# Kernel tuning notes

Measured on AMD Instinct MI355X. Metric: run time of the kernel, lower is better.

Reference implementation:

```python
import jax, jax.numpy as jnp
import numpy as np

DEPTH_REF = jnp.array([28.01, 16.32], dtype=jnp.float32)
DIM_REF = jnp.array([[3.88, 1.63, 1.53], [0.84, 1.76, 0.66], [1.78, 1.52, 1.78]], dtype=jnp.float32)
TOPK = 50
DET_THRESHOLD = 0.25
PI = 3.14159265358979


def nms_hm(heat, kernel=3):
    # 3x3 max-pool NMS: keep peaks, zero everything else
    pad = (kernel - 1) // 2
    hmax = jax.lax.reduce_window(heat, -jnp.inf, jax.lax.max,
                                 (1, 1, kernel, kernel), (1, 1, 1, 1),
                                 [(0, 0), (0, 0), (pad, pad), (pad, pad)])
    return jnp.where(hmax == heat, heat, 0.0)


def select_topk(heat, K):
    B, C, H, W = heat.shape
    scores_all, inds_all = jax.lax.top_k(heat.reshape(B, C, H * W), K)  # [B,C,K]
    ys_all = (inds_all // W).astype(jnp.float32)
    xs_all = (inds_all % W).astype(jnp.float32)
    scores, inds = jax.lax.top_k(scores_all.reshape(B, C * K), K)       # [B,K] over classes
    clses = (inds // K).astype(jnp.float32)
    topk_inds = jnp.take_along_axis(inds_all.reshape(B, C * K), inds, axis=1)
    ys = jnp.take_along_axis(ys_all.reshape(B, C * K), inds, axis=1)
    xs = jnp.take_along_axis(xs_all.reshape(B, C * K), inds, axis=1)
    return scores, topk_inds, clses, ys, xs


def select_point_of_interest(index, feature_maps):
    B, Cf, H, W = feature_maps.shape
    fm = feature_maps.transpose(0, 2, 3, 1).reshape(B, H * W, Cf)
    return jnp.take_along_axis(fm, index[:, :, None], axis=1)  # [B,K,Cf]


def encode_box3d(rotys, dims, locs):
    # dims = (l, h, w); corner signs reproduce SMOKE's gather pattern
    N = rotys.shape[0]
    c, s = jnp.cos(rotys), jnp.sin(rotys)
    z, o = jnp.zeros_like(c), jnp.ones_like(c)
    ry = jnp.stack([c, z, s, z, o, z, -s, z, c], axis=1).reshape(N, 3, 3)
    sx = jnp.array([-0.5, 0.5, 0.5, 0.5, 0.5, -0.5, -0.5, -0.5], dtype=dims.dtype)
    sy = jnp.array([-1., -1., 0., 0., -1., -1., 0., 0.], dtype=dims.dtype)
    sz = jnp.array([-0.5, -0.5, -0.5, 0.5, 0.5, 0.5, 0.5, -0.5], dtype=dims.dtype)
    corners = jnp.stack([dims[:, 0:1] * sx, dims[:, 1:2] * sy, dims[:, 2:3] * sz], axis=1)  # [N,3,8]
    return jnp.einsum('nij,njk->nik', ry, corners) + locs[:, :, None]


def setup_inputs() -> dict:
    key = jax.random.key(0)
    k1, k2 = jax.random.split(key)
    B, C, H, W = 32, 3, 192, 640
    IMG_W, IMG_H = 4 * W, 4 * H
    pred_heatmap = jax.random.uniform(k1, (B, C, H, W), dtype=jnp.float32)
    pred_regression = jax.random.normal(k2, (B, 8, H, W), dtype=jnp.float32) * 0.5
    # affine image->heatmap (scale 1/4), invertible
    tm = jnp.array([[0.25, 0., 0.], [0., 0.25, 0.], [0., 0., 1.]], dtype=jnp.float32)
    trans_mat = jnp.tile(tm[None], (B, 1, 1))
    Kc = jnp.array([[721.5, 0., IMG_W / 2.], [0., 721.5, IMG_H / 2.], [0., 0., 1.]], dtype=jnp.float32)
    K_mat = jnp.tile(Kc[None], (B, 1, 1))
    img_size = jnp.tile(jnp.array([[IMG_W, IMG_H]], dtype=jnp.float32), (B, 1))
    return {"pred_heatmap": pred_heatmap, "pred_regression": pred_regression,
            "trans_mat": trans_mat, "K_mat": K_mat, "img_size": img_size}


def reference(pred_heatmap, pred_regression, trans_mat, K_mat, img_size):
    B = pred_heatmap.shape[0]
    heat = nms_hm(pred_heatmap)
    scores, inds, clses, ys, xs = select_topk(heat, TOPK)
    reg = select_point_of_interest(inds, pred_regression).reshape(-1, 8)  # [B*K,8]

    points = jnp.stack([xs.reshape(-1), ys.reshape(-1)], axis=1)          # heatmap coords
    depth_off, proj_off = reg[:, 0], reg[:, 1:3]
    dim_off, ori = reg[:, 3:6], reg[:, 6:8]
    cls_idx = clses.reshape(-1).astype(jnp.int32)

    obj_id = jnp.repeat(jnp.arange(B), TOPK)
    tm_inv = jnp.linalg.inv(trans_mat)[obj_id]   # [N,3,3]
    K_inv = jnp.linalg.inv(K_mat)[obj_id]

    # decode location: heatmap -> image -> camera frame
    proj = points + proj_off
    proj_ext = jnp.concatenate([proj, jnp.ones_like(proj[:, :1])], axis=1)
    proj_img = jnp.einsum('nij,nj->ni', tm_inv, proj_ext)                 # image-plane homog coords
    depths = depth_off * DEPTH_REF[1] + DEPTH_REF[0]
    locs = jnp.einsum('nij,nj->ni', K_inv, proj_img * depths[:, None])

    dims = jnp.exp(dim_off) * DIM_REF[cls_idx]                            # (l,h,w)
    locs = locs.at[:, 1].add(dims[:, 1] / 2)

    # decode orientation
    eps = 1e-7
    rays = jnp.arctan(locs[:, 0] / (locs[:, 2] + eps))
    alphas = jnp.arctan(ori[:, 0] / (ori[:, 1] + eps))
    alphas = jnp.where(ori[:, 1] >= 0, alphas - PI / 2, alphas + PI / 2)
    rotys = alphas + rays
    wrap = lambda a: jnp.where(a > PI, a - 2 * PI, jnp.where(a < -PI, a + 2 * PI, a))
    rotys, alphas = wrap(rotys), wrap(alphas)

    # encode 2D boxes from projected 3D corners
    corners = encode_box3d(rotys, dims, locs)                             # [N,3,8]
    proj2 = jnp.einsum('nij,njk->nik', K_mat[obj_id], corners)
    xy = proj2[:, :2] / proj2[:, 2:3]
    Wi, Hi = img_size[obj_id, 0], img_size[obj_id, 1]
    xmins = jnp.clip(xy[:, 0].min(axis=1), 0.0, Wi)
    ymins = jnp.clip(xy[:, 1].min(axis=1), 0.0, Hi)
    xmaxs = jnp.clip(xy[:, 0].max(axis=1), 0.0, Wi)
    ymaxs = jnp.clip(xy[:, 1].max(axis=1), 0.0, Hi)
    box2d = jnp.stack([xmins, ymins, xmaxs, ymaxs], axis=1)

    dims_rolled = jnp.roll(dims, -1, axis=1)                              # (h,w,l)
    result = jnp.concatenate([
        cls_idx.astype(jnp.float32)[:, None], alphas[:, None], box2d,
        dims_rolled, locs, rotys[:, None], scores.reshape(-1, 1)], axis=1)  # [B*K,14]
    keep = result[:, -1] > DET_THRESHOLD
    return jnp.where(keep[:, None], result, 0.0)
```

## Files before the change

kernel.cpp:

```cpp
#include <hip/hip_runtime.h>
#include <math.h>

#define Hd 192
#define Wd 640
#define HWp (Hd * Wd)
#define NCLS 3
#define KTOP 50
#define NB 32
#define NPL (NB * NCLS)
#define GPR 160
#define GPP (HWp / 4)
#define SEGBLK 120
#define SEGCAP 32
#define CAP 2048
#define RBK 256
#define PI_F 3.14159265358979f

template <typename F>
__device__ inline void peaks_in_group(const float* __restrict__ p, int g, F&& f) {
  const int y = g / GPR;
  const int x0 = (g - y * GPR) * 4;
  const float* rm = p + y * Wd + x0;
  const float4 mq = *(const float4*)rm;
  const float ml = (x0 > 0) ? rm[-1] : -INFINITY;
  const float mr = (x0 + 4 < Wd) ? rm[4] : -INFINITY;
  float4 tq; float tl, tr;
  if (y > 0) {
    const float* rt = rm - Wd;
    tq = *(const float4*)rt;
    tl = (x0 > 0) ? rt[-1] : -INFINITY;
    tr = (x0 + 4 < Wd) ? rt[4] : -INFINITY;
  } else {
    tq.x = tq.y = tq.z = tq.w = -INFINITY; tl = -INFINITY; tr = -INFINITY;
  }
  float4 bq; float bl, br;
  if (y < Hd - 1) {
    const float* rb = rm + Wd;
    bq = *(const float4*)rb;
    bl = (x0 > 0) ? rb[-1] : -INFINITY;
    br = (x0 + 4 < Wd) ? rb[4] : -INFINITY;
  } else {
    bq.x = bq.y = bq.z = bq.w = -INFINITY; bl = -INFINITY; br = -INFINITY;
  }
  const float c0 = fmaxf(fmaxf(tl, ml), bl);
  const float c1 = fmaxf(fmaxf(tq.x, mq.x), bq.x);
  const float c2 = fmaxf(fmaxf(tq.y, mq.y), bq.y);
  const float c3 = fmaxf(fmaxf(tq.z, mq.z), bq.z);
  const float c4 = fmaxf(fmaxf(tq.w, mq.w), bq.w);
  const float c5 = fmaxf(fmaxf(tr, mr), br);
  const int base = y * Wd + x0;
  if (mq.x == fmaxf(fmaxf(c0, c1), c2)) f(__float_as_uint(mq.x), base + 0);
  if (mq.y == fmaxf(fmaxf(c1, c2), c3)) f(__float_as_uint(mq.y), base + 1);
  if (mq.z == fmaxf(fmaxf(c2, c3), c4)) f(__float_as_uint(mq.z), base + 2);
  if (mq.w == fmaxf(fmaxf(c3, c4), c5)) f(__float_as_uint(mq.w), base + 3);
}

template <typename F>
__device__ inline void for_each_peak_plane(const float* __restrict__ p, int tid,
                                           int nth, F&& f) {
  for (int g = tid; g < GPP; g += nth) peaks_in_group(p, g, f);
}

__device__ inline unsigned long long mk_key(unsigned int bits, int idx) {
  return ((unsigned long long)bits << 32) | (unsigned int)~idx;
}

__device__ inline int bucket_of(unsigned int bits) {
  const unsigned int base = __float_as_uint(0.995f);
  if (bits <= base) return 0;
  unsigned int d = (bits - base) >> 9;
  return d > 255u ? 255 : (int)d;
}

__global__ __launch_bounds__(256) void scan_kernel(
    const float* __restrict__ heat,
    int* __restrict__ counts,
    unsigned long long* __restrict__ segkey) {
  const int blk = blockIdx.x;
  const int plane = blk / SEGBLK;
  const int sub = blk - plane * SEGBLK;
  __shared__ unsigned long long s_k[SEGCAP];
  __shared__ int s_n;
  if (threadIdx.x == 0) s_n = 0;
  __syncthreads();

  const float* p = heat + (size_t)plane * HWp;
  const int g = sub * 256 + threadIdx.x;
  const unsigned int TB = __float_as_uint(0.995f);
  peaks_in_group(p, g, [&](unsigned int bits, int idx) {
    if (bits >= TB) {
      int slot = atomicAdd(&s_n, 1);
      if (slot < SEGCAP) s_k[slot] = mk_key(bits, idx);
    }
  });
  __syncthreads();
  const int n = s_n;
  if (threadIdx.x == 0) counts[blk] = n;
  const int nn = n < SEGCAP ? n : SEGCAP;
  if (threadIdx.x < nn)
    segkey[(size_t)blk * SEGCAP + threadIdx.x] = s_k[threadIdx.x];
}

__device__ inline void inv3(const float* m, float* o) {
  float a = m[0], b = m[1], c = m[2];
  float d = m[3], e = m[4], f = m[5];
  float g = m[6], h = m[7], i = m[8];
  float A = e * i - f * h;
  float B = -(d * i - f * g);
  float C = d * h - e * g;
  float det = a * A + b * B + c * C;
  float id = 1.0f / det;
  o[0] = A * id;            o[1] = -(b * i - c * h) * id; o[2] = (b * f - c * e) * id;
  o[3] = B * id;            o[4] = (a * i - c * g) * id;  o[5] = -(a * f - c * d) * id;
  o[6] = C * id;            o[7] = -(a * h - b * g) * id; o[8] = (a * e - b * d) * id;
}

__device__ inline float wrap_pi(float a) {
  if (a > PI_F) return a - 2.0f * PI_F;
  if (a < -PI_F) return a + 2.0f * PI_F;
  return a;
}

__constant__ float DIM_REF_C[9] = {3.88f, 1.63f, 1.53f,
                                   0.84f, 1.76f, 0.66f,
                                   1.78f, 1.52f, 1.78f};

__global__ __launch_bounds__(256) void rank_decode_kernel(
    const float* __restrict__ heat,
    const int* __restrict__ counts,
    const unsigned long long* __restrict__ segkey,
    const float* __restrict__ regr,
    const float* __restrict__ trans_mat,
    const float* __restrict__ K_mat,
    const float* __restrict__ img_size,
    float* __restrict__ out) {
  const int b = blockIdx.x;
  const int tid = threadIdx.x;

  __shared__ unsigned long long s_key[CAP];
  __shared__ unsigned long long g_key[CAP];
  __shared__ int s_off[SEGBLK + 1];
  __shared__ int cnt[RBK], suf[RBK], cur[RBK];
  __shared__ unsigned int fb_hist[1024];
  __shared__ float cls_sc[NCLS * KTOP];
  __shared__ int cls_pi[NCLS * KTOP];
  __shared__ int sel[KTOP];
  __shared__ int s_flag, s_cnt, s_B, s_above, s_T;

  for (int c = 0; c < NCLS; ++c) {
    const int plane = b * NCLS + c;
    __syncthreads();
    if (tid == 0) { s_flag = 0; s_off[0] = 0; }
    __syncthreads();
    if (tid < SEGBLK) {
      int n = counts[plane * SEGBLK + tid];
      if (n > SEGCAP) { atomicOr(&s_flag, 1); n = SEGCAP; }
      s_off[tid + 1] = n;
    }
    __syncthreads();
    if (tid == 0) {
      int acc = 0;
      for (int i = 1; i <= SEGBLK; ++i) { acc += s_off[i]; s_off[i] = acc; }
    }
    __syncthreads();
    int M = s_off[SEGBLK];
    const bool fast = (s_flag == 0) && (M >= KTOP) && (M <= CAP);

    if (fast) {
      if (tid < SEGBLK) {
        const int o = s_off[tid];
        const int n = s_off[tid + 1] - o;
        const unsigned long long* sk = segkey + (size_t)(plane * SEGBLK + tid) * SEGCAP;
        for (int i = 0; i < n; ++i) s_key[o + i] = sk[i];
      }
      __syncthreads();
    } else {
      const float* p = heat + (size_t)plane * HWp;
      for (int i = tid; i < 1024; i += 256) fb_hist[i] = 0;
      __syncthreads();
      for_each_peak_plane(p, tid, 256, [&](unsigned int bits, int idx) {
        unsigned int bkt = bits >> 20; if (bkt > 1023u) bkt = 1023u;
        atomicAdd(&fb_hist[bkt], 1u);
      });
      __syncthreads();
      if (tid == 0) {
        int acc = 0, Bs = -1;
        for (int bkt = 1023; bkt >= 0; --bkt) {
          int cc = (int)fb_hist[bkt];
          if (acc + cc >= KTOP) { Bs = bkt; s_above = acc; break; }
          acc += cc;
        }
        s_B = Bs;
        if (Bs < 0) s_above = acc;
      }
      __syncthreads();
      const int Bs = s_B;
      unsigned int T;
      if (Bs < 0) {
        T = 0;
      } else {
        for (int i = tid; i < 1024; i += 256) fb_hist[i] = 0;
        __syncthreads();
        for_each_peak_plane(p, tid, 256, [&](unsigned int bits, int idx) {
          unsigned int bkt = bits >> 20; if (bkt > 1023u) bkt = 1023u;
          if ((int)bkt == Bs) atomicAdd(&fb_hist[(bits >> 10) & 1023], 1u);
        });
        __syncthreads();
        if (tid == 0) {
          int acc = s_above, Ss = 0;
          for (int sb = 1023; sb >= 0; --sb) {
            int cc = (int)fb_hist[sb];
            if (acc + cc >= KTOP) { Ss = sb; break; }
            acc += cc;
          }
          s_T = (int)(((unsigned int)Bs << 20) | ((unsigned int)Ss << 10));
        }
        __syncthreads();
        T = (unsigned int)s_T;
      }
      if (tid == 0) s_cnt = 0;
      __syncthreads();
      for_each_peak_plane(p, tid, 256, [&](unsigned int bits, int idx) {
        if (bits >= T) {
          int slot = atomicAdd(&s_cnt, 1);
          if (slot < CAP) s_key[slot] = mk_key(bits, idx);
        }
      });
      __syncthreads();
      M = s_cnt < CAP ? s_cnt : CAP;
    }

    for (int i = tid; i < RBK; i += 256) { cnt[i] = 0; cur[i] = 0; }
    __syncthreads();
    for (int i = tid; i < M; i += 256)
      atomicAdd(&cnt[bucket_of((unsigned int)(s_key[i] >> 32))], 1);
    __syncthreads();
    if (tid == 0) {
      int acc = 0;
      for (int bq = RBK - 1; bq >= 0; --bq) { suf[bq] = acc; acc += cnt[bq]; }
    }
    __syncthreads();
    for (int i = tid; i < M; i += 256) {
      const unsigned long long k = s_key[i];
      const int bq = bucket_of((unsigned int)(k >> 32));
      const int slot = suf[bq] + atomicAdd(&cur[bq], 1);
      g_key[slot] = k;
    }
    __syncthreads();
    for (int i = tid; i < M; i += 256) {
      const unsigned long long k = g_key[i];
      const int bq = bucket_of((unsigned int)(k >> 32));
      const int st = suf[bq];
      const int nb = cnt[bq];
      int rank = st;
      for (int t = st; t < st + nb; ++t) rank += (g_key[t] > k);
      if (rank < KTOP) {
        cls_sc[c * KTOP + rank] = __uint_as_float((unsigned int)(k >> 32));
        cls_pi[c * KTOP + rank] = (int)~((unsigned int)k);
      }
    }
    for (int s2 = M + tid; s2 < KTOP; s2 += 256) {
      cls_sc[c * KTOP + s2] = 0.0f;
      cls_pi[c * KTOP + s2] = 0;
    }
  }
  __syncthreads();

  if (tid < NCLS * KTOP) {
    const float v = cls_sc[tid];
    int rank = 0;
    for (int j = 0; j < NCLS * KTOP; ++j) {
      const float w = cls_sc[j];
      rank += (w > v) || (w == v && j < tid);
    }
    if (rank < KTOP) sel[rank] = tid;
  }
  __syncthreads();

  if (tid < KTOP) {
    const int i = sel[tid];
    const int cls = i / KTOP;
    const float score = cls_sc[i];
    const int ind = cls_pi[i];
    const float ys = (float)(ind / Wd);
    const float xs = (float)(ind - (ind / Wd) * Wd);

    const float* rb = regr + (size_t)b * 8 * HWp + ind;
    const float r0 = rb[0 * HWp], r1 = rb[1 * HWp], r2 = rb[2 * HWp], r3 = rb[3 * HWp];
    const float r4 = rb[4 * HWp], r5 = rb[5 * HWp], r6 = rb[6 * HWp], r7 = rb[7 * HWp];

    float tm[9], km[9], tmi[9], kmi[9];
#pragma unroll
    for (int q = 0; q < 9; ++q) { tm[q] = trans_mat[b * 9 + q]; km[q] = K_mat[b * 9 + q]; }
    inv3(tm, tmi);
    inv3(km, kmi);

    const float px = xs + r1, py = ys + r2;
    const float gx = tmi[0] * px + tmi[1] * py + tmi[2];
    const float gy = tmi[3] * px + tmi[4] * py + tmi[5];
    const float gz = tmi[6] * px + tmi[7] * py + tmi[8];
    const float depth = r0 * 16.32f + 28.01f;
    const float qx = gx * depth, qy = gy * depth, qz = gz * depth;
    const float lx = kmi[0] * qx + kmi[1] * qy + kmi[2] * qz;
    float ly = kmi[3] * qx + kmi[4] * qy + kmi[5] * qz;
    const float lz = kmi[6] * qx + kmi[7] * qy + kmi[8] * qz;

    const float d0 = expf(r3) * DIM_REF_C[cls * 3 + 0];
    const float d1 = expf(r4) * DIM_REF_C[cls * 3 + 1];
    const float d2 = expf(r5) * DIM_REF_C[cls * 3 + 2];
    ly += d1 * 0.5f;

    const float ray = atanf(lx / (lz + 1e-7f));
    float alpha = atanf(r6 / (r7 + 1e-7f));
    alpha += (r7 >= 0.0f) ? -PI_F * 0.5f : PI_F * 0.5f;
    const float roty = wrap_pi(alpha + ray);
    alpha = wrap_pi(alpha);

    const float SX[8] = {-0.5f, 0.5f, 0.5f, 0.5f, 0.5f, -0.5f, -0.5f, -0.5f};
    const float SY[8] = {-1.0f, -1.0f, 0.0f, 0.0f, -1.0f, -1.0f, 0.0f, 0.0f};
    const float SZ[8] = {-0.5f, -0.5f, -0.5f, 0.5f, 0.5f, 0.5f, 0.5f, -0.5f};
    const float cr = cosf(roty), sr = sinf(roty);
    float minx = INFINITY, maxx = -INFINITY, miny = INFINITY, maxy = -INFINITY;
#pragma unroll
    for (int j = 0; j < 8; ++j) {
      const float ax = d0 * SX[j], ay = d1 * SY[j], az = d2 * SZ[j];
      const float cx = cr * ax + sr * az + lx;
      const float cy = ay + ly;
      const float cz = -sr * ax + cr * az + lz;
      const float ppx = km[0] * cx + km[1] * cy + km[2] * cz;
      const float ppy = km[3] * cx + km[4] * cy + km[5] * cz;
      const float ppz = km[6] * cx + km[7] * cy + km[8] * cz;
      const float X = ppx / ppz, Y = ppy / ppz;
      minx = fminf(minx, X); maxx = fmaxf(maxx, X);
      miny = fminf(miny, Y); maxy = fmaxf(maxy, Y);
    }
    const float Wi = img_size[b * 2 + 0], Hi = img_size[b * 2 + 1];
    const float xmin = fminf(fmaxf(minx, 0.0f), Wi);
    const float ymin = fminf(fmaxf(miny, 0.0f), Hi);
    const float xmax = fminf(fmaxf(maxx, 0.0f), Wi);
    const float ymax = fminf(fmaxf(maxy, 0.0f), Hi);

    float* o = out + (size_t)(b * KTOP + tid) * 14;
    if (score > 0.25f) {
      o[0] = (float)cls; o[1] = alpha;
      o[2] = xmin; o[3] = ymin; o[4] = xmax; o[5] = ymax;
      o[6] = d1; o[7] = d2; o[8] = d0;
      o[9] = lx; o[10] = ly; o[11] = lz;
      o[12] = roty; o[13] = score;
    } else {
#pragma unroll
      for (int q = 0; q < 14; ++q) o[q] = 0.0f;
    }
  }
}


extern "C" void kernel_launch(void* const* d_in, const int* in_sizes, int n_in,
                              void* d_out, int out_size, void* d_ws, size_t ws_size,
                              hipStream_t stream) {
  const float* heat = (const float*)d_in[0];
  const float* regr = (const float*)d_in[1];
  const float* tmat = (const float*)d_in[2];
  const float* kmat = (const float*)d_in[3];
  const float* isz = (const float*)d_in[4];

  char* ws = (char*)d_ws;
  int* counts = (int*)ws;
  unsigned long long* segkey = (unsigned long long*)(ws + 46080);

  scan_kernel<<<NPL * SEGBLK, 256, 0, stream>>>(heat, counts, segkey);
  rank_decode_kernel<<<NB, 256, 0, stream>>>(heat, counts, segkey,
                                             regr, tmat, kmat, isz, (float*)d_out);
}
```

Before: 226.6 us.

## Scan 16-wide strips per thread and parallelize segment key compaction

The scan kernel now has each thread handle a 16-pixel strip instead of a 4-pixel group. Neighbouring column maxima are shared across the strip, and the threshold test is checked before the peak comparison. This cuts the block count from 120 to 30 per plane and raises the per-segment capacity to 64. The rank kernel copies segment keys using all threads in a strided loop instead of one serial loop per segment. In exchange, each thread uses more registers and fewer blocks are launched, and a denser segment is more likely to overflow into the slow fallback path.

```diff
diff --git a/kernel.cpp b/kernel.cpp
--- a/kernel.cpp
+++ b/kernel.cpp
@@ -10,11 +10,17 @@
 #define NPL (NB * NCLS)
 #define GPR 160
 #define GPP (HWp / 4)
-#define SEGBLK 120
-#define SEGCAP 32
+#define SPR 40
+#define SPP (Hd * SPR)
+#define SEGBLK 30
+#define SEGCAP 64
 #define CAP 2048
 #define RBK 256
 #define PI_F 3.14159265358979f
+
+__device__ inline float fmax3(float a, float b, float c) {
+  return fmaxf(fmaxf(a, b), c);
+}
 
 template <typename F>
 __device__ inline void peaks_in_group(const float* __restrict__ p, int g, F&& f) {
@@ -42,17 +48,17 @@
   } else {
     bq.x = bq.y = bq.z = bq.w = -INFINITY; bl = -INFINITY; br = -INFINITY;
   }
-  const float c0 = fmaxf(fmaxf(tl, ml), bl);
-  const float c1 = fmaxf(fmaxf(tq.x, mq.x), bq.x);
-  const float c2 = fmaxf(fmaxf(tq.y, mq.y), bq.y);
-  const float c3 = fmaxf(fmaxf(tq.z, mq.z), bq.z);
-  const float c4 = fmaxf(fmaxf(tq.w, mq.w), bq.w);
-  const float c5 = fmaxf(fmaxf(tr, mr), br);
+  const float c0 = fmax3(tl, ml, bl);
+  const float c1 = fmax3(tq.x, mq.x, bq.x);
+  const float c2 = fmax3(tq.y, mq.y, bq.y);
+  const float c3 = fmax3(tq.z, mq.z, bq.z);
+  const float c4 = fmax3(tq.w, mq.w, bq.w);
+  const float c5 = fmax3(tr, mr, br);
   const int base = y * Wd + x0;
-  if (mq.x == fmaxf(fmaxf(c0, c1), c2)) f(__float_as_uint(mq.x), base + 0);
-  if (mq.y == fmaxf(fmaxf(c1, c2), c3)) f(__float_as_uint(mq.y), base + 1);
-  if (mq.z == fmaxf(fmaxf(c2, c3), c4)) f(__float_as_uint(mq.z), base + 2);
-  if (mq.w == fmaxf(fmaxf(c3, c4), c5)) f(__float_as_uint(mq.w), base + 3);
+  if (mq.x == fmax3(c0, c1, c2)) f(__float_as_uint(mq.x), base + 0);
+  if (mq.y == fmax3(c1, c2, c3)) f(__float_as_uint(mq.y), base + 1);
+  if (mq.z == fmax3(c2, c3, c4)) f(__float_as_uint(mq.z), base + 2);
+  if (mq.w == fmax3(c3, c4, c5)) f(__float_as_uint(mq.w), base + 3);
 }
 
 template <typename F>
@@ -70,6 +76,37 @@
   if (bits <= base) return 0;
   unsigned int d = (bits - base) >> 9;
   return d > 255u ? 255 : (int)d;
+}
+
+struct Row16 {
+  float4 q0, q1, q2, q3;
+  float l, r;
+};
+
+__device__ inline Row16 load_row16(const float* __restrict__ rp, int x0, bool valid) {
+  Row16 o;
+  if (valid) {
+    o.q0 = *(const float4*)(rp);
+    o.q1 = *(const float4*)(rp + 4);
+    o.q2 = *(const float4*)(rp + 8);
+    o.q3 = *(const float4*)(rp + 12);
+    o.l = (x0 > 0) ? rp[-1] : -INFINITY;
+    o.r = (x0 + 16 < Wd) ? rp[16] : -INFINITY;
+  } else {
+    o.q0.x = o.q0.y = o.q0.z = o.q0.w = -INFINITY;
+    o.q1 = o.q0; o.q2 = o.q0; o.q3 = o.q0;
+    o.l = -INFINITY; o.r = -INFINITY;
+  }
+  return o;
+}
+
+__device__ inline float4 max3v(const float4 a, const float4 b, const float4 c) {
+  float4 o;
+  o.x = fmax3(a.x, b.x, c.x);
+  o.y = fmax3(a.y, b.y, c.y);
+  o.z = fmax3(a.z, b.z, c.z);
+  o.w = fmax3(a.w, b.w, c.w);
+  return o;
 }
 
 __global__ __launch_bounds__(256) void scan_kernel(
@@ -84,15 +121,47 @@
   if (threadIdx.x == 0) s_n = 0;
   __syncthreads();
 
-  const float* p = heat + (size_t)plane * HWp;
-  const int g = sub * 256 + threadIdx.x;
-  const unsigned int TB = __float_as_uint(0.995f);
-  peaks_in_group(p, g, [&](unsigned int bits, int idx) {
-    if (bits >= TB) {
-      int slot = atomicAdd(&s_n, 1);
-      if (slot < SEGCAP) s_k[slot] = mk_key(bits, idx);
-    }
-  });
+  const int strip = sub * 256 + threadIdx.x;
+  const int y = strip / SPR;
+  const int x0 = (strip - y * SPR) * 16;
+  const float* pm = heat + (size_t)plane * HWp + y * Wd + x0;
+
+  const Row16 m = load_row16(pm, x0, true);
+  const Row16 t = load_row16(pm - Wd, x0, y > 0);
+  const Row16 b = load_row16(pm + Wd, x0, y < Hd - 1);
+
+  const float cl = fmax3(t.l, m.l, b.l);
+  const float cr = fmax3(t.r, m.r, b.r);
+  const float4 c0 = max3v(t.q0, m.q0, b.q0);
+  const float4 c1 = max3v(t.q1, m.q1, b.q1);
+  const float4 c2 = max3v(t.q2, m.q2, b.q2);
+  const float4 c3 = max3v(t.q3, m.q3, b.q3);
+
+  const float TH = 0.995f;
+  const int base = y * Wd + x0;
+#define EMIT(V, W0, W1, W2, J)                                         \
+  if ((V) >= TH && (V) == fmax3((W0), (W1), (W2))) {                   \
+    int slot = atomicAdd(&s_n, 1);                                     \
+    if (slot < SEGCAP) s_k[slot] = mk_key(__float_as_uint(V), base + (J)); \
+  }
+  EMIT(m.q0.x, cl,   c0.x, c0.y, 0)
+  EMIT(m.q0.y, c0.x, c0.y, c0.z, 1)
+  EMIT(m.q0.z, c0.y, c0.z, c0.w, 2)
+  EMIT(m.q0.w, c0.z, c0.w, c1.x, 3)
+  EMIT(m.q1.x, c0.w, c1.x, c1.y, 4)
+  EMIT(m.q1.y, c1.x, c1.y, c1.z, 5)
+  EMIT(m.q1.z, c1.y, c1.z, c1.w, 6)
+  EMIT(m.q1.w, c1.z, c1.w, c2.x, 7)
+  EMIT(m.q2.x, c1.w, c2.x, c2.y, 8)
+  EMIT(m.q2.y, c2.x, c2.y, c2.z, 9)
+  EMIT(m.q2.z, c2.y, c2.z, c2.w, 10)
+  EMIT(m.q2.w, c2.z, c2.w, c3.x, 11)
+  EMIT(m.q3.x, c2.w, c3.x, c3.y, 12)
+  EMIT(m.q3.y, c3.x, c3.y, c3.z, 13)
+  EMIT(m.q3.z, c3.y, c3.z, c3.w, 14)
+  EMIT(m.q3.w, c3.z, c3.w, cr,   15)
+#undef EMIT
+
   __syncthreads();
   const int n = s_n;
   if (threadIdx.x == 0) counts[blk] = n;
@@ -167,11 +236,13 @@
     const bool fast = (s_flag == 0) && (M >= KTOP) && (M <= CAP);
 
     if (fast) {
-      if (tid < SEGBLK) {
-        const int o = s_off[tid];
-        const int n = s_off[tid + 1] - o;
-        const unsigned long long* sk = segkey + (size_t)(plane * SEGBLK + tid) * SEGCAP;
-        for (int i = 0; i < n; ++i) s_key[o + i] = sk[i];
+      const unsigned long long* pk = segkey + (size_t)plane * SEGBLK * SEGCAP;
+      for (int i = tid; i < SEGBLK * SEGCAP; i += 256) {
+        const int s = i >> 6;
+        const int j = i & (SEGCAP - 1);
+        const int o = s_off[s];
+        const int n = s_off[s + 1] - o;
+        if (j < n) s_key[o + j] = pk[(size_t)s * SEGCAP + j];
       }
       __syncthreads();
     } else {
@@ -366,7 +437,7 @@
 
   char* ws = (char*)d_ws;
   int* counts = (int*)ws;
-  unsigned long long* segkey = (unsigned long long*)(ws + 46080);
+  unsigned long long* segkey = (unsigned long long*)(ws + NPL * SEGBLK * 4);
 
   scan_kernel<<<NPL * SEGBLK, 256, 0, stream>>>(heat, counts, segkey);
   rank_decode_kernel<<<NB, 256, 0, stream>>>(heat, counts, segkey,
```

Measured after the change: 230.6 us. Within noise of the previous version (+1.8%).
